# Performance work log

Hardware: AMD Instinct MI355X
Metric: run time of the kernel (lower is better)

Reference implementation:

```python
import jax, jax.numpy as jnp
import numpy as np

N_NODES = 50000
N_EDGES = 625000
F_IN = 128
F_OUT = 128


def setup_inputs() -> dict:
    key = jax.random.key(0)
    k_x, k_w, k_v, k_r, k_c = jax.random.split(key, 5)
    # Xavier-uniform bound for weight init (matches nn.init.xavier_uniform_)
    bound = float(np.sqrt(6.0 / (F_IN + F_OUT)))
    return {
        "x": jax.random.normal(k_x, (N_NODES, F_IN), dtype=jnp.float32),
        "weight": jax.random.uniform(k_w, (F_IN, F_OUT), minval=-bound, maxval=bound, dtype=jnp.float32),
        "bias": jnp.zeros((F_OUT,), dtype=jnp.float32),
        "edge_vals": jax.random.uniform(k_v, (N_EDGES,), dtype=jnp.float32),
        "edge_rows": jax.random.randint(k_r, (N_EDGES,), 0, N_NODES, dtype=jnp.int32),
        "edge_cols": jax.random.randint(k_c, (N_EDGES,), 0, N_NODES, dtype=jnp.int32),
    }


def reference(x, weight, bias, edge_vals, edge_rows, edge_cols):
    # support = input @ weight  (dense GEMM)  -> [N, F_out]
    support = x @ weight
    # output = spmm(adj, support): for each edge (r, c, v): out[r] += v * support[c]
    msgs = support[edge_cols] * edge_vals[:, None]          # [E, F_out] gather
    out = jax.ops.segment_sum(msgs, edge_rows, num_segments=N_NODES)  # scatter-add
    return out + bias
```

## Files before the change

### kernel.cpp

```cpp
#include <hip/hip_runtime.h>
#include <hip/hip_bf16.h>


#define F_DIM 128

#define NBC 98
#define SLABC 7360
#define NROW_PAD (NBC * 512)

#define BIN_T 256
#define BIN_EPT 8
#define BIN_CHUNK (BIN_T * BIN_EPT)

#define SPLIT_T 512
#define SPLIT_EPT 15

typedef short bf16x8 __attribute__((ext_vector_type(8)));
typedef float f32x4 __attribute__((ext_vector_type(4)));

__device__ __forceinline__ unsigned short f2bf(float f) {
    unsigned int u = __float_as_uint(f);
    u += 0x7FFFu + ((u >> 16) & 1u);
    return (unsigned short)(u >> 16);
}

__global__ void __launch_bounds__(BIN_T)
k1_kernel(const int* __restrict__ rows, const int* __restrict__ cols,
          const float* __restrict__ vals, int* __restrict__ lenC,
          uint2* __restrict__ ebinC, int n_edges,
          const float* __restrict__ w, unsigned short* __restrict__ wt,
          int nbin) {
    __shared__ int lcnt[NBC];
    __shared__ int lbase[NBC];
    __shared__ int garr[NBC];
    __shared__ int w0sum;
    __shared__ uint2 srec[BIN_CHUNK];
    __shared__ unsigned char sbkt[BIN_CHUNK];

    const int t = threadIdx.x;

    if ((int)blockIdx.x >= nbin) {
        int idx = (blockIdx.x - nbin) * BIN_T + t;
        int n = idx >> 7, k = idx & 127;
        wt[n * F_DIM + k] = f2bf(w[k * F_DIM + n]);
        return;
    }

    const int base = blockIdx.x * BIN_CHUNK;

    if (t < NBC) lcnt[t] = 0;
    __syncthreads();

    unsigned int mykey[BIN_EPT];
    float myval[BIN_EPT];
    bool myok[BIN_EPT];
#pragma unroll
    for (int j = 0; j < BIN_EPT; j++) {
        int e = base + j * BIN_T + t;
        myok[j] = (e < n_edges);
        if (myok[j]) {
            int r = rows[e];
            int c = cols[e];
            myval[j] = vals[e];
            mykey[j] = ((unsigned)r << 16) | (unsigned)c;
            atomicAdd(&lcnt[r >> 9], 1);
        }
    }
    __syncthreads();

    const int lane = t & 63;
    int cval = 0, inc = 0;
    if (t < 128) {
        cval = (t < NBC) ? lcnt[t] : 0;
        inc = cval;
#pragma unroll
        for (int d = 1; d < 64; d <<= 1) {
            int u = __shfl_up(inc, d);
            if (lane >= d) inc += u;
        }
        if (t == 63) w0sum = inc;
    }
    __syncthreads();
    if (t >= 64 && t < 128) inc += w0sum;
    if (t < NBC) {
        int lb = inc - cval;
        lbase[t] = lb;
        if (cval > 0) garr[t] = t * SLABC + atomicAdd(&lenC[t], cval);
        lcnt[t] = lb;
    }
    __syncthreads();

#pragma unroll
    for (int j = 0; j < BIN_EPT; j++) {
        if (myok[j]) {
            int b = (int)(mykey[j] >> 25);
            int p = atomicAdd(&lcnt[b], 1);
            srec[p] = make_uint2(mykey[j], __float_as_uint(myval[j]));
            sbkt[p] = (unsigned char)b;
        }
    }
    __syncthreads();

    const int m = min(BIN_CHUNK, n_edges - base);
    for (int i = t; i < m; i += BIN_T) {
        int b = sbkt[i];
        int dst = garr[b] + (i - lbase[b]);
        if (dst < (b + 1) * SLABC) ebinC[dst] = srec[i];
    }
}

__global__ void __launch_bounds__(SPLIT_T)
split_kernel(const int* __restrict__ lenC, const uint2* __restrict__ ebinC,
             uint2* __restrict__ ebin2, int* __restrict__ roff,
             int* __restrict__ rlen) {
    __shared__ int cnt[SPLIT_T];
    __shared__ int lb[SPLIT_T];
    __shared__ int pos[SPLIT_T];
    __shared__ int wsum[8], wbase[8];
    __shared__ uint2 srec[SLABC];

    const int b = blockIdx.x;
    const int t = threadIdx.x;
    const int n = min(lenC[b], SLABC);
    const uint2* src = ebinC + (size_t)b * SLABC;

    cnt[t] = 0;
    __syncthreads();

    uint2 myr[SPLIT_EPT];
    int myrow[SPLIT_EPT];
#pragma unroll
    for (int j = 0; j < SPLIT_EPT; j++) {
        int idx = j * SPLIT_T + t;
        myrow[j] = -1;
        if (idx < n) {
            myr[j] = src[idx];
            myrow[j] = (int)((myr[j].x >> 16) & 511u);
            atomicAdd(&cnt[myrow[j]], 1);
        }
    }
    __syncthreads();

    const int lane = t & 63;
    const int wv = t >> 6;
    const int myc = cnt[t];
    int inc = myc;
#pragma unroll
    for (int d = 1; d < 64; d <<= 1) {
        int u = __shfl_up(inc, d);
        if (lane >= d) inc += u;
    }
    if (lane == 63) wsum[wv] = inc;
    __syncthreads();
    if (t == 0) {
        int run = 0;
#pragma unroll
        for (int k = 0; k < 8; k++) { wbase[k] = run; run += wsum[k]; }
    }
    __syncthreads();
    const int excl = wbase[wv] + inc - myc;
    lb[t] = excl;
    pos[t] = excl;
    __syncthreads();

#pragma unroll
    for (int j = 0; j < SPLIT_EPT; j++) {
        if (myrow[j] >= 0) {
            int p = atomicAdd(&pos[myrow[j]], 1);
            srec[p] = myr[j];
        }
    }
    __syncthreads();

    const int gbase = b * SLABC;
    for (int i = t; i < n; i += SPLIT_T)
        ebin2[gbase + i] = srec[i];
    roff[(b << 9) + t] = gbase + lb[t];
    rlen[(b << 9) + t] = myc;
}

__global__ void __launch_bounds__(256)
gemm_mfma_kernel(const float* __restrict__ x, const unsigned short* __restrict__ wt,
                 unsigned short* __restrict__ support) {
    const int tid = threadIdx.x;
    const int wid = tid >> 6;
    const int lane = tid & 63;
    const int l15 = lane & 15;
    const int lhi = lane >> 4;

    const int m0 = blockIdx.x * 16;
    const int n0 = wid * 32;

    const float* xrow = x + (size_t)(m0 + l15) * F_DIM + lhi * 8;
    const unsigned short* wrow0 = wt + (size_t)(n0 + l15) * F_DIM + lhi * 8;
    const unsigned short* wrow1 = wrow0 + 16 * F_DIM;

    f32x4 acc0 = {0.f, 0.f, 0.f, 0.f};
    f32x4 acc1 = {0.f, 0.f, 0.f, 0.f};
#pragma unroll
    for (int k0 = 0; k0 < F_DIM; k0 += 32) {
        float4 xa = *reinterpret_cast<const float4*>(xrow + k0);
        float4 xb = *reinterpret_cast<const float4*>(xrow + k0 + 4);
        bf16x8 a, b0, b1;
        a[0] = (short)f2bf(xa.x); a[1] = (short)f2bf(xa.y);
        a[2] = (short)f2bf(xa.z); a[3] = (short)f2bf(xa.w);
        a[4] = (short)f2bf(xb.x); a[5] = (short)f2bf(xb.y);
        a[6] = (short)f2bf(xb.z); a[7] = (short)f2bf(xb.w);
        b0 = *reinterpret_cast<const bf16x8*>(wrow0 + k0);
        b1 = *reinterpret_cast<const bf16x8*>(wrow1 + k0);
        acc0 = __builtin_amdgcn_mfma_f32_16x16x32_bf16(a, b0, acc0, 0, 0, 0);
        acc1 = __builtin_amdgcn_mfma_f32_16x16x32_bf16(a, b1, acc1, 0, 0, 0);
    }

    unsigned short* sp = support + (size_t)(m0 + 4 * lhi) * F_DIM + n0 + l15;
#pragma unroll
    for (int i = 0; i < 4; i++) {
        sp[(size_t)i * F_DIM]      = f2bf(acc0[i]);
        sp[(size_t)i * F_DIM + 16] = f2bf(acc1[i]);
    }
}

__global__ void __launch_bounds__(256)
bspmm_kernel(const unsigned short* __restrict__ support,
             const uint2* __restrict__ ebin2, const int* __restrict__ roff,
             const int* __restrict__ rlen, const float* __restrict__ bias,
             float* __restrict__ out, int n_nodes) {
    const int row = blockIdx.x * 4 + (threadIdx.x >> 6);
    const int lane = threadIdx.x & 63;
    const int half = lane >> 5;
    const int l32 = lane & 31;
    const unsigned coff = l32 * 4u;
    if (row >= n_nodes) return;

    const int s = roff[row];
    const int n = rlen[row];

    float a0 = 0.f, a1 = 0.f, a2 = 0.f, a3 = 0.f;

#define GATH(K) (*reinterpret_cast<const uint2*>(                             \
        support + (size_t)((K) & 0xffffu) * F_DIM + coff))
#define ACC4(VAL, SV)                                                         \
    {                                                                         \
        float v = __uint_as_float(VAL);                                       \
        a0 += v * __uint_as_float((SV).x << 16);                              \
        a1 += v * __uint_as_float((SV).x & 0xFFFF0000u);                      \
        a2 += v * __uint_as_float((SV).y << 16);                              \
        a3 += v * __uint_as_float((SV).y & 0xFFFF0000u);                      \
    }

    int i = 0;
#pragma unroll 1
    for (; i + 7 < n; i += 8) {
        const int j = s + i + half;
        uint2 r0 = ebin2[j];
        uint2 r1 = ebin2[j + 2];
        uint2 r2 = ebin2[j + 4];
        uint2 r3 = ebin2[j + 6];
        uint2 s0 = GATH(r0.x);
        uint2 s1 = GATH(r1.x);
        uint2 s2 = GATH(r2.x);
        uint2 s3 = GATH(r3.x);
        ACC4(r0.y, s0) ACC4(r1.y, s1) ACC4(r2.y, s2) ACC4(r3.y, s3)
    }
#pragma unroll 1
    for (; i + 1 < n; i += 2) {
        uint2 r = ebin2[s + i + half];
        uint2 sv = GATH(r.x);
        ACC4(r.y, sv)
    }
    if (i < n && half == 0) {
        uint2 r = ebin2[s + i];
        uint2 sv = GATH(r.x);
        ACC4(r.y, sv)
    }
#undef GATH
#undef ACC4

    a0 += __shfl_xor(a0, 32);
    a1 += __shfl_xor(a1, 32);
    a2 += __shfl_xor(a2, 32);
    a3 += __shfl_xor(a3, 32);

    if (half == 0) {
        const float4 bb = *reinterpret_cast<const float4*>(bias + coff);
        float4 o = make_float4(a0 + bb.x, a1 + bb.y, a2 + bb.z, a3 + bb.w);
        *reinterpret_cast<float4*>(out + (size_t)row * F_DIM + coff) = o;
    }
}

extern "C" void kernel_launch(void* const* d_in, const int* in_sizes, int n_in,
                              void* d_out, int out_size, void* d_ws, size_t ws_size,
                              hipStream_t stream) {
    const float* x      = (const float*)d_in[0];
    const float* weight = (const float*)d_in[1];
    const float* bias   = (const float*)d_in[2];
    const float* evals  = (const float*)d_in[3];
    const int*   erows  = (const int*)d_in[4];
    const int*   ecols  = (const int*)d_in[5];
    float* out = (float*)d_out;

    const int n_nodes = in_sizes[0] / F_DIM;
    const int n_edges = in_sizes[3];

    unsigned short* support = (unsigned short*)d_ws;
    unsigned short* wt      = support + (size_t)n_nodes * F_DIM;
    int* lenC = (int*)(wt + F_DIM * F_DIM);
    int* roff = lenC + 128;
    int* rlen = roff + NROW_PAD;
    uintptr_t ep = (uintptr_t)(rlen + NROW_PAD);
    ep = (ep + 15) & ~(uintptr_t)15;
    uint2* ebinC = (uint2*)ep;
    uint2* ebin2 = ebinC + (size_t)NBC * SLABC;

    hipMemsetAsync(lenC, 0, NBC * sizeof(int), stream);

    int nbin = (n_edges + BIN_CHUNK - 1) / BIN_CHUNK;
    k1_kernel<<<nbin + 64, BIN_T, 0, stream>>>(erows, ecols, evals, lenC,
                                               ebinC, n_edges, weight, wt, nbin);

    split_kernel<<<NBC, SPLIT_T, 0, stream>>>(lenC, ebinC, ebin2, roff, rlen);

    gemm_mfma_kernel<<<n_nodes / 16, 256, 0, stream>>>(x, wt, support);

    bspmm_kernel<<<(n_nodes + 3) / 4, 256, 0, stream>>>(support, ebin2, roff,
                                                        rlen, bias, out, n_nodes);
}
```

Baseline: 90.03 us.

## Fuse GEMM into split kernel and move weight transpose into init kernel

The dense GEMM blocks now launch as extra blocks of the split kernel, so the underfilled 98-block split pass overlaps with the support computation. The weight transpose and lenC zeroing move into a small init kernel that replaces the memset, which leaves the binning kernel with only edge blocks. The cost is that GEMM blocks run at 512 threads and carry the split kernel's large static shared-memory footprint, which may reduce occupancy for the GEMM part.

```diff
diff --git a/kernel.cpp b/kernel.cpp
--- a/kernel.cpp
+++ b/kernel.cpp
@@ -14,6 +14,7 @@
 
 #define SPLIT_T 512
 #define SPLIT_EPT 15
+#define GEMM_BLKS 1563
 
 typedef short bf16x8 __attribute__((ext_vector_type(8)));
 typedef float f32x4 __attribute__((ext_vector_type(4)));
@@ -24,12 +25,22 @@
     return (unsigned short)(u >> 16);
 }
 
+__global__ void __launch_bounds__(256)
+init_kernel(const float* __restrict__ w, unsigned short* __restrict__ wt,
+            int* __restrict__ lenC) {
+    if (blockIdx.x == 64) {
+        if (threadIdx.x < NBC) lenC[threadIdx.x] = 0;
+        return;
+    }
+    int idx = blockIdx.x * 256 + threadIdx.x;
+    int n = idx >> 7, k = idx & 127;
+    wt[n * F_DIM + k] = f2bf(w[k * F_DIM + n]);
+}
+
 __global__ void __launch_bounds__(BIN_T)
 k1_kernel(const int* __restrict__ rows, const int* __restrict__ cols,
           const float* __restrict__ vals, int* __restrict__ lenC,
-          uint2* __restrict__ ebinC, int n_edges,
-          const float* __restrict__ w, unsigned short* __restrict__ wt,
-          int nbin) {
+          uint2* __restrict__ ebinC, int n_edges) {
     __shared__ int lcnt[NBC];
     __shared__ int lbase[NBC];
     __shared__ int garr[NBC];
@@ -38,14 +49,6 @@
     __shared__ unsigned char sbkt[BIN_CHUNK];
 
     const int t = threadIdx.x;
-
-    if ((int)blockIdx.x >= nbin) {
-        int idx = (blockIdx.x - nbin) * BIN_T + t;
-        int n = idx >> 7, k = idx & 127;
-        wt[n * F_DIM + k] = f2bf(w[k * F_DIM + n]);
-        return;
-    }
-
     const int base = blockIdx.x * BIN_CHUNK;
 
     if (t < NBC) lcnt[t] = 0;
@@ -110,17 +113,67 @@
 }
 
 __global__ void __launch_bounds__(SPLIT_T)
-split_kernel(const int* __restrict__ lenC, const uint2* __restrict__ ebinC,
-             uint2* __restrict__ ebin2, int* __restrict__ roff,
-             int* __restrict__ rlen) {
+splitgemm_kernel(const int* __restrict__ lenC, const uint2* __restrict__ ebinC,
+                 uint2* __restrict__ ebin2, int* __restrict__ roff,
+                 int* __restrict__ rlen,
+                 const float* __restrict__ x, const unsigned short* __restrict__ wt,
+                 unsigned short* __restrict__ support, int n_nodes) {
     __shared__ int cnt[SPLIT_T];
     __shared__ int lb[SPLIT_T];
     __shared__ int pos[SPLIT_T];
     __shared__ int wsum[8], wbase[8];
     __shared__ uint2 srec[SLABC];
 
+    const int t = threadIdx.x;
+
+    if ((int)blockIdx.x >= NBC) {
+        const int gb = blockIdx.x - NBC;
+        const int wid = t >> 6;
+        const int mt = wid >> 2;
+        const int nw = wid & 3;
+        const int lane = t & 63;
+        const int l15 = lane & 15;
+        const int lhi = lane >> 4;
+
+        const int m0 = gb * 32 + mt * 16;
+        const int n0 = nw * 32;
+
+        int xr = m0 + l15;
+        if (xr >= n_nodes) xr = n_nodes - 1;
+        const float* xrow = x + (size_t)xr * F_DIM + lhi * 8;
+        const unsigned short* wrow0 = wt + (size_t)(n0 + l15) * F_DIM + lhi * 8;
+        const unsigned short* wrow1 = wrow0 + 16 * F_DIM;
+
+        f32x4 acc0 = {0.f, 0.f, 0.f, 0.f};
+        f32x4 acc1 = {0.f, 0.f, 0.f, 0.f};
+#pragma unroll
+        for (int k0 = 0; k0 < F_DIM; k0 += 32) {
+            float4 xa = *reinterpret_cast<const float4*>(xrow + k0);
+            float4 xb = *reinterpret_cast<const float4*>(xrow + k0 + 4);
+            bf16x8 a, b0, b1;
+            a[0] = (short)f2bf(xa.x); a[1] = (short)f2bf(xa.y);
+            a[2] = (short)f2bf(xa.z); a[3] = (short)f2bf(xa.w);
+            a[4] = (short)f2bf(xb.x); a[5] = (short)f2bf(xb.y);
+            a[6] = (short)f2bf(xb.z); a[7] = (short)f2bf(xb.w);
+            b0 = *reinterpret_cast<const bf16x8*>(wrow0 + k0);
+            b1 = *reinterpret_cast<const bf16x8*>(wrow1 + k0);
+            acc0 = __builtin_amdgcn_mfma_f32_16x16x32_bf16(a, b0, acc0, 0, 0, 0);
+            acc1 = __builtin_amdgcn_mfma_f32_16x16x32_bf16(a, b1, acc1, 0, 0, 0);
+        }
+
+        unsigned short* sp = support + (size_t)(m0 + 4 * lhi) * F_DIM + n0 + l15;
+#pragma unroll
+        for (int i = 0; i < 4; i++) {
+            int row = m0 + 4 * lhi + i;
+            if (row < n_nodes) {
+                sp[(size_t)i * F_DIM]      = f2bf(acc0[i]);
+                sp[(size_t)i * F_DIM + 16] = f2bf(acc1[i]);
+            }
+        }
+        return;
+    }
+
     const int b = blockIdx.x;
-    const int t = threadIdx.x;
     const int n = min(lenC[b], SLABC);
     const uint2* src = ebinC + (size_t)b * SLABC;
 
@@ -177,47 +230,6 @@
         ebin2[gbase + i] = srec[i];
     roff[(b << 9) + t] = gbase + lb[t];
     rlen[(b << 9) + t] = myc;
-}
-
-__global__ void __launch_bounds__(256)
-gemm_mfma_kernel(const float* __restrict__ x, const unsigned short* __restrict__ wt,
-                 unsigned short* __restrict__ support) {
-    const int tid = threadIdx.x;
-    const int wid = tid >> 6;
-    const int lane = tid & 63;
-    const int l15 = lane & 15;
-    const int lhi = lane >> 4;
-
-    const int m0 = blockIdx.x * 16;
-    const int n0 = wid * 32;
-
-    const float* xrow = x + (size_t)(m0 + l15) * F_DIM + lhi * 8;
-    const unsigned short* wrow0 = wt + (size_t)(n0 + l15) * F_DIM + lhi * 8;
-    const unsigned short* wrow1 = wrow0 + 16 * F_DIM;
-
-    f32x4 acc0 = {0.f, 0.f, 0.f, 0.f};
-    f32x4 acc1 = {0.f, 0.f, 0.f, 0.f};
-#pragma unroll
-    for (int k0 = 0; k0 < F_DIM; k0 += 32) {
-        float4 xa = *reinterpret_cast<const float4*>(xrow + k0);
-        float4 xb = *reinterpret_cast<const float4*>(xrow + k0 + 4);
-        bf16x8 a, b0, b1;
-        a[0] = (short)f2bf(xa.x); a[1] = (short)f2bf(xa.y);
-        a[2] = (short)f2bf(xa.z); a[3] = (short)f2bf(xa.w);
-        a[4] = (short)f2bf(xb.x); a[5] = (short)f2bf(xb.y);
-        a[6] = (short)f2bf(xb.z); a[7] = (short)f2bf(xb.w);
-        b0 = *reinterpret_cast<const bf16x8*>(wrow0 + k0);
-        b1 = *reinterpret_cast<const bf16x8*>(wrow1 + k0);
-        acc0 = __builtin_amdgcn_mfma_f32_16x16x32_bf16(a, b0, acc0, 0, 0, 0);
-        acc1 = __builtin_amdgcn_mfma_f32_16x16x32_bf16(a, b1, acc1, 0, 0, 0);
-    }
-
-    unsigned short* sp = support + (size_t)(m0 + 4 * lhi) * F_DIM + n0 + l15;
-#pragma unroll
-    for (int i = 0; i < 4; i++) {
-        sp[(size_t)i * F_DIM]      = f2bf(acc0[i]);
-        sp[(size_t)i * F_DIM + 16] = f2bf(acc1[i]);
-    }
 }
 
 __global__ void __launch_bounds__(256)
@@ -312,15 +324,14 @@
     uint2* ebinC = (uint2*)ep;
     uint2* ebin2 = ebinC + (size_t)NBC * SLABC;
 
-    hipMemsetAsync(lenC, 0, NBC * sizeof(int), stream);
+    init_kernel<<<65, 256, 0, stream>>>(weight, wt, lenC);
 
     int nbin = (n_edges + BIN_CHUNK - 1) / BIN_CHUNK;
-    k1_kernel<<<nbin + 64, BIN_T, 0, stream>>>(erows, ecols, evals, lenC,
-                                               ebinC, n_edges, weight, wt, nbin);
-
-    split_kernel<<<NBC, SPLIT_T, 0, stream>>>(lenC, ebinC, ebin2, roff, rlen);
-
-    gemm_mfma_kernel<<<n_nodes / 16, 256, 0, stream>>>(x, wt, support);
+    k1_kernel<<<nbin, BIN_T, 0, stream>>>(erows, ecols, evals, lenC,
+                                          ebinC, n_edges);
+
+    splitgemm_kernel<<<NBC + GEMM_BLKS, SPLIT_T, 0, stream>>>(
+        lenC, ebinC, ebin2, roff, rlen, x, wt, support, n_nodes);
 
     bspmm_kernel<<<(n_nodes + 3) / 4, 256, 0, stream>>>(support, ebin2, roff,
                                                         rlen, bias, out, n_nodes);
```

Result: faster. 81.48 us (-9.5%).
